# Kernel tuning notes

Measured on AMD Instinct MI355X. Metric: run time of the kernel, lower is better.

The kernel has to match this reference:

```python
import jax, jax.numpy as jnp
import numpy as np

H, NH, HD = 1024, 16, 64
B, T, S = 2, 1024, 3
NOISE, STEP, TEMP, NSTEPS = 0.1, 0.01, 1.0, 5
LN_EPS = 1e-5


def setup_inputs() -> dict:
    key = jax.random.key(0)
    ks = jax.random.split(key, 9)
    return {
        "queries": jax.random.normal(ks[0], (B, NH, T, HD), jnp.float32),
        "keys": jax.random.normal(ks[1], (B, NH, T, HD), jnp.float32),
        "values": jax.random.normal(ks[2], (B, NH, T, HD), jnp.float32),
        "hidden_states": jax.random.normal(ks[3], (B, T, H), jnp.float32),
        "W1": jax.random.normal(ks[4], (H, H), jnp.float32) * 0.02,
        "b1": jnp.zeros((H,), jnp.float32),
        "ln_g": jnp.ones((H,), jnp.float32),
        "ln_b": jnp.zeros((H,), jnp.float32),
        "W2": jax.random.normal(ks[5], (H, H), jnp.float32) * 0.02,
        "b2": jnp.zeros((H,), jnp.float32),
        "hyp_noise": jax.random.normal(ks[6], (S, B, NH, T, HD), jnp.float32),
        "ref_noise": jax.random.normal(ks[7], (S, NSTEPS - 1, B, NH, T, HD), jnp.float32),
    }


def _attention_energy(q, k, v):
    # q: [S,B,H,T,D]; k,v: [B,H,T,D] -> energy [S,B]
    scores = jnp.einsum('sbhtd,bhud->sbhtu', q, k) / jnp.sqrt(jnp.float32(q.shape[-1]))
    attn = jax.nn.softmax(scores, axis=-1)
    out = jnp.einsum('sbhtu,bhud->sbhtd', attn, v)
    out_mag = jnp.linalg.norm(out, axis=-1).mean(axis=(2, 3))          # [S,B]
    entropy = -(attn * jnp.log(attn + 1e-8)).sum(axis=-1).mean(axis=(2, 3))
    align = (q * k[None]).sum(axis=-1).mean(axis=(2, 3))
    return out_mag - 0.1 * entropy - 0.05 * align


def reference(queries, keys, values, hidden_states, W1, b1, ln_g, ln_b, W2, b2,
              hyp_noise, ref_noise):
    # query_predictor: Linear -> LayerNorm -> ReLU -> Linear
    x = hidden_states @ W1.T + b1
    mu = x.mean(axis=-1, keepdims=True)
    var = ((x - mu) ** 2).mean(axis=-1, keepdims=True)
    x = (x - mu) / jnp.sqrt(var + LN_EPS) * ln_g + ln_b
    x = jax.nn.relu(x)
    ctx = x @ W2.T + b2                                   # [B,T,H]
    ctx = ctx.reshape(B, T, NH, HD).transpose(0, 2, 1, 3) # [B,NH,T,HD]

    # exploration hypotheses, refined jointly over the sample axis
    q = queries[None] + hyp_noise * NOISE                 # [S,B,NH,T,HD]
    for step in range(NSTEPS):
        q = q - STEP * (q - ctx[None])                    # PCN prediction-error update
        if step < NSTEPS - 1:
            q = q + ref_noise[:, step] * 0.01

    energies = _attention_energy(q, keys, values)         # [S,B]
    probs = jax.nn.softmax(-energies / TEMP, axis=0)      # [S,B]
    selected = jnp.einsum('sb,sbhtd->bhtd', probs, q)     # softmax-weighted mix
    return selected, keys, values
```

## Files before the change

kernel.cpp:

```cpp
#include <hip/hip_runtime.h>
#include <hip/hip_bf16.h>
#include <math.h>

#define NB 2
#define NHH 16
#define TT 1024
#define HDD 64
#define NSS 3
#define HH 1024

typedef float f4 __attribute__((ext_vector_type(4)));
typedef short bf16x8 __attribute__((ext_vector_type(8)));
typedef unsigned short u16;
typedef u16 u16x4 __attribute__((ext_vector_type(4)));

__device__ inline u16 f2bf(float f) {
    union { float f; unsigned u; } v; v.f = f;
    unsigned r = (v.u + 0x7FFFu + ((v.u >> 16) & 1u)) >> 16;
    return (u16)r;
}
__device__ inline float bf2f(u16 u) {
    union { unsigned u; float f; } v; v.u = ((unsigned)u) << 16;
    return v.f;
}
__device__ inline unsigned cvtpk(float lo, float hi) {
    unsigned r;
    asm("v_cvt_pk_bf16_f32 %0, %1, %2" : "=v"(r) : "v"(lo), "v"(hi));
    return r;
}
__device__ inline void gl_lds16(const u16* g, u16* l) {
    __builtin_amdgcn_global_load_lds(
        (const __attribute__((address_space(1))) unsigned int*)g,
        (__attribute__((address_space(3))) unsigned int*)l, 16, 0, 0);
}

__device__ inline float red16sum(float v) {
    v += __shfl_xor(v, 1);
    v += __shfl_xor(v, 2);
    v += __shfl_xor(v, 4);
    v += __shfl_xor(v, 8);
    return v;
}
__device__ inline float red64sum(float v) {
    v += __shfl_xor(v, 1);
    v += __shfl_xor(v, 2);
    v += __shfl_xor(v, 4);
    v += __shfl_xor(v, 8);
    v += __shfl_xor(v, 16);
    v += __shfl_xor(v, 32);
    return v;
}

__global__ __launch_bounds__(256) void k_prep(const float* __restrict__ hs, u16* __restrict__ hs_b,
                                              const float* __restrict__ W1, u16* __restrict__ w1_b,
                                              const float* __restrict__ W2, u16* __restrict__ w2_b,
                                              const float* __restrict__ keys, u16* __restrict__ k_b,
                                              float* __restrict__ outk,
                                              const float* __restrict__ V, u16* __restrict__ vt_b,
                                              float* __restrict__ outv) {
    __shared__ float tile[64][65];
    int b = blockIdx.x;
    if (b < 4096) {
        const float* s; u16* d; int base;
        if (b < 2048)      { s = hs; d = hs_b; base = 0; }
        else if (b < 3072) { s = W1; d = w1_b; base = 2048; }
        else               { s = W2; d = w2_b; base = 3072; }
        int i = (b - base) * 256 + threadIdx.x;
        f4 v = ((const f4*)s)[i];
        u16x4 o;
        o[0] = f2bf(v[0]); o[1] = f2bf(v[1]); o[2] = f2bf(v[2]); o[3] = f2bf(v[3]);
        ((u16x4*)d)[i] = o;
        return;
    }
    if (b < 5120) {
        int c = (b - 4096) * 256 + threadIdx.x;
        int bh = c >> 13, t = (c >> 3) & 1023, col8 = c & 7;
        int kt = t >> 6, row = t & 63;
        const float* sp = keys + (size_t)c * 8;
        f4 v0 = *(const f4*)(sp);
        f4 v1 = *(const f4*)(sp + 4);
        *(f4*)(outk + (size_t)c * 8) = v0;
        *(f4*)(outk + (size_t)c * 8 + 4) = v1;
        union { unsigned u[4]; int4 i4; } o;
        o.u[0] = cvtpk(v0[0] * 0.125f, v0[1] * 0.125f);
        o.u[1] = cvtpk(v0[2] * 0.125f, v0[3] * 0.125f);
        o.u[2] = cvtpk(v1[0] * 0.125f, v1[1] * 0.125f);
        o.u[3] = cvtpk(v1[2] * 0.125f, v1[3] * 0.125f);
        *(int4*)(k_b + (size_t)(bh * 16 + kt) * 4096 + row * 64 + ((col8 ^ (row & 7)) << 3)) = o.i4;
        return;
    }
    int idx = b - 5120;
    int bh = idx >> 4, kt = idx & 15, t0 = kt * 64;
    int r = threadIdx.x >> 2, c0 = (threadIdx.x & 3) * 16;
    const float* vp = V + ((size_t)bh * TT + t0) * HDD;
#pragma unroll
    for (int j = 0; j < 16; j += 4) {
        f4 v = *(const f4*)(vp + r * HDD + c0 + j);
        tile[r][c0 + j + 0] = v[0]; tile[r][c0 + j + 1] = v[1];
        tile[r][c0 + j + 2] = v[2]; tile[r][c0 + j + 3] = v[3];
        *(f4*)(outv + ((size_t)bh * TT + t0 + r) * HDD + c0 + j) = v;
    }
    __syncthreads();
    int d = threadIdx.x >> 2, x0 = (threadIdx.x & 3) * 16;
    u16* op = vt_b + (size_t)(bh * 16 + kt) * 4096 + d * 64;
#pragma unroll
    for (int cc = 0; cc < 2; ++cc) {
        int c8 = (x0 >> 3) + cc;
        union { unsigned u[4]; int4 i4; } o;
#pragma unroll
        for (int p = 0; p < 4; ++p)
            o.u[p] = cvtpk(tile[c8 * 8 + 2 * p][d], tile[c8 * 8 + 2 * p + 1][d]);
        *(int4*)(op + ((c8 ^ (d & 7)) << 3)) = o.i4;
    }
}

template <int EPI>
__global__ __launch_bounds__(256) void k_gemm_bt(const u16* __restrict__ A,
                                                 const u16* __restrict__ Bm,
                                                 const float* __restrict__ bias,
                                                 const float* __restrict__ que,
                                                 void* __restrict__ outv) {
    const int K = 1024, N = 1024;
    int w = threadIdx.x >> 6, l = threadIdx.x & 63, lr = l & 15, lg = l >> 4;
    int m0 = blockIdx.y * 64 + w * 16;
    int n0 = blockIdx.x * 64;
    const u16* ap = A + (size_t)(m0 + lr) * K + lg * 8;
    const u16* bp = Bm + (size_t)(n0 + lr) * K + lg * 8;
    f4 z4 = {0.f, 0.f, 0.f, 0.f};
    f4 acc[4] = {z4, z4, z4, z4};
#pragma unroll 2
    for (int kk = 0; kk < K; kk += 32) {
        bf16x8 a  = *(const bf16x8*)(ap + kk);
        bf16x8 b0 = *(const bf16x8*)(bp + kk);
        bf16x8 b1 = *(const bf16x8*)(bp + 16 * K + kk);
        bf16x8 b2 = *(const bf16x8*)(bp + 32 * K + kk);
        bf16x8 b3 = *(const bf16x8*)(bp + 48 * K + kk);
        acc[0] = __builtin_amdgcn_mfma_f32_16x16x32_bf16(a, b0, acc[0], 0, 0, 0);
        acc[1] = __builtin_amdgcn_mfma_f32_16x16x32_bf16(a, b1, acc[1], 0, 0, 0);
        acc[2] = __builtin_amdgcn_mfma_f32_16x16x32_bf16(a, b2, acc[2], 0, 0, 0);
        acc[3] = __builtin_amdgcn_mfma_f32_16x16x32_bf16(a, b3, acc[3], 0, 0, 0);
    }
    const float A5 = 0.9509900499f, CC = 1.0f - A5;
#pragma unroll
    for (int cf = 0; cf < 4; ++cf) {
        int col = n0 + cf * 16 + lr;
        float bs = bias[col];
#pragma unroll
        for (int r = 0; r < 4; ++r) {
            int row = m0 + lg * 4 + r;
            float v = acc[cf][r] + bs;
            if (EPI == 0) {
                ((u16*)outv)[(size_t)row * N + col] = f2bf(v);
            } else {
                int b = row >> 10, t = row & 1023, nh = col >> 6, hd = col & 63;
                size_t oidx = (((size_t)(b * NHH + nh)) * TT + t) * HDD + hd;
                ((float*)outv)[oidx] = A5 * que[oidx] + CC * v;
            }
        }
    }
}

__global__ __launch_bounds__(256) void k_lnrelu(const u16* __restrict__ X,
                                                const float* __restrict__ g,
                                                const float* __restrict__ bta,
                                                u16* __restrict__ xr) {
    int row = blockIdx.x;
    u16x4 xv = ((const u16x4*)(X + (size_t)row * HH))[threadIdx.x];
    f4 v;
    v[0] = bf2f(xv[0]); v[1] = bf2f(xv[1]); v[2] = bf2f(xv[2]); v[3] = bf2f(xv[3]);
    float s = v[0] + v[1] + v[2] + v[3];
    float s2 = v[0] * v[0] + v[1] * v[1] + v[2] * v[2] + v[3] * v[3];
    s = red64sum(s);
    s2 = red64sum(s2);
    __shared__ float red[8];
    int w = threadIdx.x >> 6, l = threadIdx.x & 63;
    if (l == 0) { red[w] = s; red[w + 4] = s2; }
    __syncthreads();
    float S1 = red[0] + red[1] + red[2] + red[3];
    float S2 = red[4] + red[5] + red[6] + red[7];
    float mu = S1 * (1.0f / 1024.0f);
    float var = S2 * (1.0f / 1024.0f) - mu * mu;
    float rstd = rsqrtf(var + 1e-5f);
    f4 gv = ((const f4*)g)[threadIdx.x];
    f4 bv = ((const f4*)bta)[threadIdx.x];
    u16x4 o;
#pragma unroll
    for (int j = 0; j < 4; ++j) {
        float y = (v[j] - mu) * rstd * gv[j] + bv[j];
        y = fmaxf(y, 0.f);
        o[j] = f2bf(y);
    }
    ((u16x4*)(xr + (size_t)row * HH))[threadIdx.x] = o;
}

__global__ __launch_bounds__(256, 3) void k_attn(const float* __restrict__ basep_,
                                                 const float* __restrict__ hyp,
                                                 const float* __restrict__ rn,
                                                 const u16* __restrict__ Kb,
                                                 const u16* __restrict__ Vt,
                                                 u16* __restrict__ qq,
                                                 float* __restrict__ part) {
    int bi = blockIdx.x;
    int p_ = bi & 31, j_ = bi >> 5;
    int h = p_ & 15, b = p_ >> 4;
    int s = j_ >> 3, qt2 = j_ & 7;
    int sb = s * 2 + b;
    int bh = b * NHH + h;
    int pi = sb * 128 + h * 8 + qt2;
    int w = threadIdx.x >> 6, l = threadIdx.x & 63, lr = l & 15, lg = l >> 4;
    int t0 = qt2 * 128;
    f4 z4 = {0.f, 0.f, 0.f, 0.f};

    __shared__ u16 Ks[2][4096];
    __shared__ u16 Vs[2][4096];
    __shared__ u16 plds[8][1024];

    const u16* kT = Kb + (size_t)(bh * 16) * 4096;
    const u16* vT = Vt + (size_t)(bh * 16) * 4096;

#pragma unroll
    for (int j = 0; j < 2; ++j) {
        int co = (w + 4 * j) * 512;
        gl_lds16(kT + co + l * 8, &Ks[0][co]);
        gl_lds16(vT + co + l * 8, &Vs[0][co]);
    }

    const float CH = 0.1f * 0.9509900499f;
    const float C0 = 0.0096059601f, C1 = 0.0097029900f, C2 = 0.0098010000f, C3 = 0.0099f;
    const float* basep = basep_ + ((size_t)bh * TT) * HDD;
    const float* hypp = hyp + ((size_t)(sb * NHH + h) * TT) * HDD;
    const float* rn0p = rn + ((size_t)(((s * 4 + 0) * 2 + b) * NHH + h) * TT) * HDD;
    const float* rn1p = rn + ((size_t)(((s * 4 + 1) * 2 + b) * NHH + h) * TT) * HDD;
    const float* rn2p = rn + ((size_t)(((s * 4 + 2) * 2 + b) * NHH + h) * TT) * HDD;
    const float* rn3p = rn + ((size_t)(((s * 4 + 3) * 2 + b) * NHH + h) * TT) * HDD;
    u16* qqp = qq + ((size_t)(sb * NHH + h) * TT) * HDD;

    char* slab = (char*)&plds[0][0];
    {
        int t = threadIdx.x;
#pragma unroll
        for (int m = 0; m < 4; ++m) {
            int j = t + 256 * m;
            size_t off = (size_t)t0 * HDD + (size_t)j * 8;
            f4 a0 = *(const f4*)(basep + off);
            f4 a1 = *(const f4*)(basep + off + 4);
            a0 += CH * __builtin_nontemporal_load((const f4*)(hypp + off));
            a1 += CH * __builtin_nontemporal_load((const f4*)(hypp + off + 4));
            a0 += C0 * __builtin_nontemporal_load((const f4*)(rn0p + off));
            a1 += C0 * __builtin_nontemporal_load((const f4*)(rn0p + off + 4));
            a0 += C1 * __builtin_nontemporal_load((const f4*)(rn1p + off));
            a1 += C1 * __builtin_nontemporal_load((const f4*)(rn1p + off + 4));
            a0 += C2 * __builtin_nontemporal_load((const f4*)(rn2p + off));
            a1 += C2 * __builtin_nontemporal_load((const f4*)(rn2p + off + 4));
            a0 += C3 * __builtin_nontemporal_load((const f4*)(rn3p + off));
            a1 += C3 * __builtin_nontemporal_load((const f4*)(rn3p + off + 4));
            union { unsigned u[4]; int4 i4; } o;
            o.u[0] = cvtpk(a0[0], a0[1]); o.u[1] = cvtpk(a0[2], a0[3]);
            o.u[2] = cvtpk(a1[0], a1[1]); o.u[3] = cvtpk(a1[2], a1[3]);
            int row = j >> 3, slot = j & 7;
            *(int4*)(slab + row * 128 + (((slot ^ (row & 7))) << 4)) = o.i4;
            *(int4*)(qqp + (size_t)t0 * HDD + (size_t)j * 8) = o.i4;
        }
    }
    __syncthreads();

    bf16x8 aq[2][2];
#pragma unroll
    for (int qr = 0; qr < 2; ++qr) {
        int r_ = w * 32 + qr * 16 + lr;
#pragma unroll
        for (int c = 0; c < 2; ++c)
            aq[qr][c] = *(const bf16x8*)(slab + r_ * 128 + (((c * 4 + lg) ^ (r_ & 7)) << 4));
    }

    f4 acco[2][4] = {{z4, z4, z4, z4}, {z4, z4, z4, z4}};
    float zrow[2][4] = {{0.f, 0.f, 0.f, 0.f}, {0.f, 0.f, 0.f, 0.f}};
    float wrow[2][4] = {{0.f, 0.f, 0.f, 0.f}, {0.f, 0.f, 0.f, 0.f}};
    float al_lane = 0.f;
    int kdiag = qt2 * 2 + (w >> 1);

    for (int kt = 0; kt < 16; ++kt) {
        int cur = kt & 1;
        if (kt < 15) {
#pragma unroll
            for (int j = 0; j < 2; ++j) {
                int co = (w + 4 * j) * 512;
                gl_lds16(kT + (kt + 1) * 4096 + co + l * 8, &Ks[cur ^ 1][co]);
                gl_lds16(vT + (kt + 1) * 4096 + co + l * 8, &Vs[cur ^ 1][co]);
            }
        }
        char* KsB = (char*)Ks[cur];
        char* VsB = (char*)Vs[cur];

        f4 sc[2][4];
        __builtin_amdgcn_s_setprio(1);
#pragma unroll
        for (int cf = 0; cf < 4; ++cf) {
            int row = cf * 16 + lr, rs = row & 7;
            bf16x8 bk0 = *(const bf16x8*)(KsB + row * 128 + ((lg ^ rs) << 4));
            bf16x8 bk1 = *(const bf16x8*)(KsB + row * 128 + (((4 + lg) ^ rs) << 4));
            f4 t0a = __builtin_amdgcn_mfma_f32_16x16x32_bf16(aq[0][0], bk0, z4, 0, 0, 0);
            sc[0][cf] = __builtin_amdgcn_mfma_f32_16x16x32_bf16(aq[0][1], bk1, t0a, 0, 0, 0);
            f4 t1a = __builtin_amdgcn_mfma_f32_16x16x32_bf16(aq[1][0], bk0, z4, 0, 0, 0);
            sc[1][cf] = __builtin_amdgcn_mfma_f32_16x16x32_bf16(aq[1][1], bk1, t1a, 0, 0, 0);
        }
        __builtin_amdgcn_s_setprio(0);

        if (kt == kdiag) {
            f4 sd0 = (w & 1) ? sc[0][2] : sc[0][0];
            f4 sd1 = (w & 1) ? sc[1][3] : sc[1][1];
            int rr = lr & 3;
            float e0 = rr == 0 ? sd0[0] : (rr == 1 ? sd0[1] : (rr == 2 ? sd0[2] : sd0[3]));
            float e1 = rr == 0 ? sd1[0] : (rr == 1 ? sd1[1] : (rr == 2 ? sd1[2] : sd1[3]));
            if (lg == (lr >> 2)) al_lane += (e0 + e1) * 8.0f;
        }

#pragma unroll
        for (int qr = 0; qr < 2; ++qr) {
            u16* pl = &plds[w * 2 + qr][0];
#pragma unroll
            for (int cf = 0; cf < 4; ++cf) {
                float p0 = __expf(sc[qr][cf][0]);
                float p1 = __expf(sc[qr][cf][1]);
                float p2 = __expf(sc[qr][cf][2]);
                float p3 = __expf(sc[qr][cf][3]);
                zrow[qr][0] += p0; zrow[qr][1] += p1;
                zrow[qr][2] += p2; zrow[qr][3] += p3;
                wrow[qr][0] = fmaf(p0, sc[qr][cf][0], wrow[qr][0]);
                wrow[qr][1] = fmaf(p1, sc[qr][cf][1], wrow[qr][1]);
                wrow[qr][2] = fmaf(p2, sc[qr][cf][2], wrow[qr][2]);
                wrow[qr][3] = fmaf(p3, sc[qr][cf][3], wrow[qr][3]);
                unsigned pa01 = cvtpk(p0, p1), pa23 = cvtpk(p2, p3);
                int base_ = cf * 16 + lr;
                pl[(((lg * 4 + 0) * 64 + base_)) ^ (((lg * 4 + 0) & 7) << 3)] = (u16)pa01;
                pl[(((lg * 4 + 1) * 64 + base_)) ^ (((lg * 4 + 1) & 7) << 3)] = (u16)(pa01 >> 16);
                pl[(((lg * 4 + 2) * 64 + base_)) ^ (((lg * 4 + 2) & 7) << 3)] = (u16)pa23;
                pl[(((lg * 4 + 3) * 64 + base_)) ^ (((lg * 4 + 3) & 7) << 3)] = (u16)(pa23 >> 16);
            }
        }
        bf16x8 pa[2][2];
#pragma unroll
        for (int qr = 0; qr < 2; ++qr) {
            const u16* pl = &plds[w * 2 + qr][0];
            pa[qr][0] = *(const bf16x8*)&pl[(lr * 64 + lg * 8) ^ ((lr & 7) << 3)];
            pa[qr][1] = *(const bf16x8*)&pl[(lr * 64 + 32 + lg * 8) ^ ((lr & 7) << 3)];
        }
        __builtin_amdgcn_s_setprio(1);
#pragma unroll
        for (int cf = 0; cf < 4; ++cf) {
            int row = cf * 16 + lr, rs = row & 7;
            bf16x8 bv0 = *(const bf16x8*)(VsB + row * 128 + ((lg ^ rs) << 4));
            bf16x8 bv1 = *(const bf16x8*)(VsB + row * 128 + (((4 + lg) ^ rs) << 4));
            acco[0][cf] = __builtin_amdgcn_mfma_f32_16x16x32_bf16(pa[0][0], bv0, acco[0][cf], 0, 0, 0);
            acco[0][cf] = __builtin_amdgcn_mfma_f32_16x16x32_bf16(pa[0][1], bv1, acco[0][cf], 0, 0, 0);
            acco[1][cf] = __builtin_amdgcn_mfma_f32_16x16x32_bf16(pa[1][0], bv0, acco[1][cf], 0, 0, 0);
            acco[1][cf] = __builtin_amdgcn_mfma_f32_16x16x32_bf16(pa[1][1], bv1, acco[1][cf], 0, 0, 0);
        }
        __builtin_amdgcn_s_setprio(0);

        __syncthreads();
    }

    float magw = 0.f, entw = 0.f;
#pragma unroll
    for (int qr = 0; qr < 2; ++qr) {
#pragma unroll
        for (int r = 0; r < 4; ++r) {
            float zz = red16sum(zrow[qr][r]);
            float ww = red16sum(wrow[qr][r]);
            float ssq = acco[qr][0][r] * acco[qr][0][r] + acco[qr][1][r] * acco[qr][1][r] +
                        acco[qr][2][r] * acco[qr][2][r] + acco[qr][3][r] * acco[qr][3][r];
            ssq = red16sum(ssq);
            float inv = 1.0f / zz;
            magw += sqrtf(ssq) * inv;
            entw += __logf(zz) - ww * inv;
        }
    }
    magw += __shfl_xor(magw, 16); magw += __shfl_xor(magw, 32);
    entw += __shfl_xor(entw, 16); entw += __shfl_xor(entw, 32);
    float al = red64sum(al_lane);

    __shared__ float red[4][3];
    if (l == 0) { red[w][0] = magw; red[w][1] = entw; red[w][2] = al; }
    __syncthreads();
    if (threadIdx.x == 0) {
        part[pi * 3 + 0] = red[0][0] + red[1][0] + red[2][0] + red[3][0];
        part[pi * 3 + 1] = red[0][1] + red[1][1] + red[2][1] + red[3][1];
        part[pi * 3 + 2] = red[0][2] + red[1][2] + red[2][2] + red[3][2];
    }
}

__global__ void k_finalize(const float* __restrict__ part, float* __restrict__ probs) {
    int w = threadIdx.x >> 6, l = threadIdx.x & 63;
    __shared__ float eng[6];
    if (w < 6) {
        float a0 = 0.f, a1 = 0.f, a2 = 0.f;
        for (int i = l; i < 128; i += 64) {
            const float* pp = part + (size_t)(w * 128 + i) * 3;
            a0 += pp[0]; a1 += pp[1]; a2 += pp[2];
        }
        a0 = red64sum(a0); a1 = red64sum(a1); a2 = red64sum(a2);
        if (l == 0) {
            const float inv = 1.0f / 16384.0f;
            eng[w] = a0 * inv - 0.1f * (a1 * inv) - 0.05f * (a2 * inv);
        }
    }
    __syncthreads();
    if (threadIdx.x < 2) {
        int b = threadIdx.x;
        float e0 = -eng[0 + b], e1 = -eng[2 + b], e2 = -eng[4 + b];
        float mx = fmaxf(e0, fmaxf(e1, e2));
        float x0 = __expf(e0 - mx), x1 = __expf(e1 - mx), x2 = __expf(e2 - mx);
        float inv = 1.0f / (x0 + x1 + x2);
        probs[0 + b] = x0 * inv;
        probs[2 + b] = x1 * inv;
        probs[4 + b] = x2 * inv;
    }
}

__global__ __launch_bounds__(256) void k_select(const u16* __restrict__ qq,
                                                const float* __restrict__ probs,
                                                float* __restrict__ out) {
    const int NQ4 = 524288;
    int i = blockIdx.x * 256 + threadIdx.x;
    int b = i >> 18;
    float p0 = probs[0 + b], p1 = probs[2 + b], p2 = probs[4 + b];
    u16x4 a0 = ((const u16x4*)qq)[i];
    u16x4 a1 = ((const u16x4*)qq)[NQ4 + i];
    u16x4 a2 = ((const u16x4*)qq)[2 * NQ4 + i];
    f4 v;
#pragma unroll
    for (int j = 0; j < 4; ++j)
        v[j] = p0 * bf2f(a0[j]) + p1 * bf2f(a1[j]) + p2 * bf2f(a2[j]);
    ((f4*)out)[i] = v;
}

extern "C" void kernel_launch(void* const* d_in, const int* in_sizes, int n_in,
                              void* d_out, int out_size, void* d_ws, size_t ws_size,
                              hipStream_t stream) {
    const float* queries = (const float*)d_in[0];
    const float* keys    = (const float*)d_in[1];
    const float* values  = (const float*)d_in[2];
    const float* hs      = (const float*)d_in[3];
    const float* W1      = (const float*)d_in[4];
    const float* b1      = (const float*)d_in[5];
    const float* ln_g    = (const float*)d_in[6];
    const float* ln_b    = (const float*)d_in[7];
    const float* W2      = (const float*)d_in[8];
    const float* b2      = (const float*)d_in[9];
    const float* hyp     = (const float*)d_in[10];
    const float* rn      = (const float*)d_in[11];
    float* out = (float*)d_out;
    char* ws = (char*)d_ws;

    const size_t MB = 1024ull * 1024ull;
    u16*   qq16 = (u16*)(ws);
    u16*   hs_b = (u16*)(ws + 0 * MB);
    u16*   w1_b = (u16*)(ws + 4 * MB);
    u16*   w2_b = (u16*)(ws + 6 * MB);
    u16*   X    = (u16*)(ws + 8 * MB);
    u16*   xr   = (u16*)(ws + 16 * MB);
    float* base = (float*)(ws + 24 * MB);
    u16*   k_b  = (u16*)(ws + 32 * MB);
    u16*   vt_b = (u16*)(ws + 36 * MB);
    float* part = (float*)(ws + 40 * MB);
    float* probs= (float*)(ws + 40 * MB + 65536);

    k_prep<<<5632, 256, 0, stream>>>(hs, hs_b, W1, w1_b, W2, w2_b,
                                     keys, k_b, out + 2097152,
                                     values, vt_b, out + 4194304);

    k_gemm_bt<0><<<dim3(16, 32), 256, 0, stream>>>(hs_b, w1_b, b1, nullptr, X);
    k_lnrelu<<<2048, 256, 0, stream>>>(X, ln_g, ln_b, xr);
    k_gemm_bt<1><<<dim3(16, 32), 256, 0, stream>>>(xr, w2_b, b2, queries, base);

    k_attn<<<768, 256, 0, stream>>>(base, hyp, rn, k_b, vt_b, qq16, part);
    k_finalize<<<1, 384, 0, stream>>>(part, probs);
    k_select<<<2048, 256, 0, stream>>>(qq16, probs, out);
}
```

Measured before the change: 167.4 us.

## Precombine noise terms in prep kernel and rebuild hypotheses from base plus noise

The five noise tensors (hyp and four ref_noise steps) are combined once in k_prep into a single bf16 noise tensor per sample. k_attn then reads base plus one bf16 noise stream instead of five fp32 streams, and no longer writes the bf16 hypothesis buffer qq. k_select rebuilds the selected output as base + sum_s p_s*noise_s, using the fact that the probabilities sum to one. The aim is to cut the heavy fp32 noise traffic inside the attention kernel and remove the qq write. The cost is extra prep work and a change in rounding, since noise is rounded to bf16 separately from base.

```diff
diff --git a/kernel.cpp b/kernel.cpp
--- a/kernel.cpp
+++ b/kernel.cpp
@@ -51,7 +51,16 @@
     return v;
 }
 
-__global__ __launch_bounds__(256) void k_prep(const float* __restrict__ hs, u16* __restrict__ hs_b,
+#define PCN_CH 0.0950990050f
+#define PCN_C0 0.0096059601f
+#define PCN_C1 0.0097029900f
+#define PCN_C2 0.0098010000f
+#define PCN_C3 0.0099000000f
+
+__global__ __launch_bounds__(256) void k_prep(const float* __restrict__ hyp,
+                                              const float* __restrict__ rn,
+                                              u16* __restrict__ noise16,
+                                              const float* __restrict__ hs, u16* __restrict__ hs_b,
                                               const float* __restrict__ W1, u16* __restrict__ w1_b,
                                               const float* __restrict__ W2, u16* __restrict__ w2_b,
                                               const float* __restrict__ keys, u16* __restrict__ k_b,
@@ -60,20 +69,51 @@
                                               float* __restrict__ outv) {
     __shared__ float tile[64][65];
     int b = blockIdx.x;
-    if (b < 4096) {
+    if (b < 1536) {
+        int sidx = b >> 9, blk = b & 511;
+        size_t so = (size_t)sidx * 2097152;
+        int o = blk * 4096 + threadIdx.x * 4;
+        const float* hp = hyp + so;
+        const float* r0 = rn + (size_t)(sidx * 4 + 0) * 2097152;
+        const float* r1 = rn + (size_t)(sidx * 4 + 1) * 2097152;
+        const float* r2 = rn + (size_t)(sidx * 4 + 2) * 2097152;
+        const float* r3 = rn + (size_t)(sidx * 4 + 3) * 2097152;
+        u16* np = noise16 + so;
+        f4 vh[4], v0[4], v1[4], v2[4], v3[4];
+#pragma unroll
+        for (int j = 0; j < 4; ++j) {
+            vh[j] = __builtin_nontemporal_load((const f4*)(hp + o + j * 1024));
+            v0[j] = __builtin_nontemporal_load((const f4*)(r0 + o + j * 1024));
+            v1[j] = __builtin_nontemporal_load((const f4*)(r1 + o + j * 1024));
+            v2[j] = __builtin_nontemporal_load((const f4*)(r2 + o + j * 1024));
+            v3[j] = __builtin_nontemporal_load((const f4*)(r3 + o + j * 1024));
+        }
+#pragma unroll
+        for (int j = 0; j < 4; ++j) {
+            f4 v = PCN_CH * vh[j] + PCN_C0 * v0[j] + PCN_C1 * v1[j] +
+                   PCN_C2 * v2[j] + PCN_C3 * v3[j];
+            unsigned pr[2];
+            pr[0] = cvtpk(v[0], v[1]);
+            pr[1] = cvtpk(v[2], v[3]);
+            *(uint2*)(np + o + j * 1024) = *(uint2*)pr;
+        }
+        return;
+    }
+    if (b < 5632) {
+        int b2 = b - 1536;
         const float* s; u16* d; int base;
-        if (b < 2048)      { s = hs; d = hs_b; base = 0; }
-        else if (b < 3072) { s = W1; d = w1_b; base = 2048; }
-        else               { s = W2; d = w2_b; base = 3072; }
-        int i = (b - base) * 256 + threadIdx.x;
+        if (b2 < 2048)      { s = hs; d = hs_b; base = 0; }
+        else if (b2 < 3072) { s = W1; d = w1_b; base = 2048; }
+        else                { s = W2; d = w2_b; base = 3072; }
+        int i = (b2 - base) * 256 + threadIdx.x;
         f4 v = ((const f4*)s)[i];
         u16x4 o;
         o[0] = f2bf(v[0]); o[1] = f2bf(v[1]); o[2] = f2bf(v[2]); o[3] = f2bf(v[3]);
         ((u16x4*)d)[i] = o;
         return;
     }
-    if (b < 5120) {
-        int c = (b - 4096) * 256 + threadIdx.x;
+    if (b < 6656) {
+        int c = (b - 5632) * 256 + threadIdx.x;
         int bh = c >> 13, t = (c >> 3) & 1023, col8 = c & 7;
         int kt = t >> 6, row = t & 63;
         const float* sp = keys + (size_t)c * 8;
@@ -89,7 +129,7 @@
         *(int4*)(k_b + (size_t)(bh * 16 + kt) * 4096 + row * 64 + ((col8 ^ (row & 7)) << 3)) = o.i4;
         return;
     }
-    int idx = b - 5120;
+    int idx = b - 6656;
     int bh = idx >> 4, kt = idx & 15, t0 = kt * 64;
     int r = threadIdx.x >> 2, c0 = (threadIdx.x & 3) * 16;
     const float* vp = V + ((size_t)bh * TT + t0) * HDD;
@@ -194,11 +234,9 @@
 }
 
 __global__ __launch_bounds__(256, 3) void k_attn(const float* __restrict__ basep_,
-                                                 const float* __restrict__ hyp,
-                                                 const float* __restrict__ rn,
+                                                 const u16* __restrict__ noise16,
                                                  const u16* __restrict__ Kb,
                                                  const u16* __restrict__ Vt,
-                                                 u16* __restrict__ qq,
                                                  float* __restrict__ part) {
     int bi = blockIdx.x;
     int p_ = bi & 31, j_ = bi >> 5;
@@ -225,15 +263,8 @@
         gl_lds16(vT + co + l * 8, &Vs[0][co]);
     }
 
-    const float CH = 0.1f * 0.9509900499f;
-    const float C0 = 0.0096059601f, C1 = 0.0097029900f, C2 = 0.0098010000f, C3 = 0.0099f;
-    const float* basep = basep_ + ((size_t)bh * TT) * HDD;
-    const float* hypp = hyp + ((size_t)(sb * NHH + h) * TT) * HDD;
-    const float* rn0p = rn + ((size_t)(((s * 4 + 0) * 2 + b) * NHH + h) * TT) * HDD;
-    const float* rn1p = rn + ((size_t)(((s * 4 + 1) * 2 + b) * NHH + h) * TT) * HDD;
-    const float* rn2p = rn + ((size_t)(((s * 4 + 2) * 2 + b) * NHH + h) * TT) * HDD;
-    const float* rn3p = rn + ((size_t)(((s * 4 + 3) * 2 + b) * NHH + h) * TT) * HDD;
-    u16* qqp = qq + ((size_t)(sb * NHH + h) * TT) * HDD;
+    const float* basep = basep_ + (size_t)bh * TT * HDD;
+    const u16* noisep = noise16 + (size_t)s * 2097152 + (size_t)bh * TT * HDD;
 
     char* slab = (char*)&plds[0][0];
     {
@@ -244,22 +275,18 @@
             size_t off = (size_t)t0 * HDD + (size_t)j * 8;
             f4 a0 = *(const f4*)(basep + off);
             f4 a1 = *(const f4*)(basep + off + 4);
-            a0 += CH * __builtin_nontemporal_load((const f4*)(hypp + off));
-            a1 += CH * __builtin_nontemporal_load((const f4*)(hypp + off + 4));
-            a0 += C0 * __builtin_nontemporal_load((const f4*)(rn0p + off));
-            a1 += C0 * __builtin_nontemporal_load((const f4*)(rn0p + off + 4));
-            a0 += C1 * __builtin_nontemporal_load((const f4*)(rn1p + off));
-            a1 += C1 * __builtin_nontemporal_load((const f4*)(rn1p + off + 4));
-            a0 += C2 * __builtin_nontemporal_load((const f4*)(rn2p + off));
-            a1 += C2 * __builtin_nontemporal_load((const f4*)(rn2p + off + 4));
-            a0 += C3 * __builtin_nontemporal_load((const f4*)(rn3p + off));
-            a1 += C3 * __builtin_nontemporal_load((const f4*)(rn3p + off + 4));
+            union { int4 i4; u16 u[8]; } nv;
+            nv.i4 = *(const int4*)(noisep + off);
+#pragma unroll
+            for (int k = 0; k < 4; ++k) {
+                a0[k] += bf2f(nv.u[k]);
+                a1[k] += bf2f(nv.u[4 + k]);
+            }
             union { unsigned u[4]; int4 i4; } o;
             o.u[0] = cvtpk(a0[0], a0[1]); o.u[1] = cvtpk(a0[2], a0[3]);
             o.u[2] = cvtpk(a1[0], a1[1]); o.u[3] = cvtpk(a1[2], a1[3]);
             int row = j >> 3, slot = j & 7;
             *(int4*)(slab + row * 128 + (((slot ^ (row & 7))) << 4)) = o.i4;
-            *(int4*)(qqp + (size_t)t0 * HDD + (size_t)j * 8) = o.i4;
         }
     }
     __syncthreads();
@@ -418,20 +445,21 @@
     }
 }
 
-__global__ __launch_bounds__(256) void k_select(const u16* __restrict__ qq,
+__global__ __launch_bounds__(256) void k_select(const float* __restrict__ base,
+                                                const u16* __restrict__ noise16,
                                                 const float* __restrict__ probs,
                                                 float* __restrict__ out) {
-    const int NQ4 = 524288;
+    const int NG = 524288;
     int i = blockIdx.x * 256 + threadIdx.x;
     int b = i >> 18;
     float p0 = probs[0 + b], p1 = probs[2 + b], p2 = probs[4 + b];
-    u16x4 a0 = ((const u16x4*)qq)[i];
-    u16x4 a1 = ((const u16x4*)qq)[NQ4 + i];
-    u16x4 a2 = ((const u16x4*)qq)[2 * NQ4 + i];
-    f4 v;
+    f4 v = ((const f4*)base)[i];
+    u16x4 n0 = ((const u16x4*)noise16)[i];
+    u16x4 n1 = ((const u16x4*)noise16)[NG + i];
+    u16x4 n2 = ((const u16x4*)noise16)[2 * NG + i];
 #pragma unroll
     for (int j = 0; j < 4; ++j)
-        v[j] = p0 * bf2f(a0[j]) + p1 * bf2f(a1[j]) + p2 * bf2f(a2[j]);
+        v[j] += p0 * bf2f(n0[j]) + p1 * bf2f(n1[j]) + p2 * bf2f(n2[j]);
     ((f4*)out)[i] = v;
 }
 
@@ -454,19 +482,20 @@
     char* ws = (char*)d_ws;
 
     const size_t MB = 1024ull * 1024ull;
-    u16*   qq16 = (u16*)(ws);
-    u16*   hs_b = (u16*)(ws + 0 * MB);
-    u16*   w1_b = (u16*)(ws + 4 * MB);
-    u16*   w2_b = (u16*)(ws + 6 * MB);
-    u16*   X    = (u16*)(ws + 8 * MB);
-    u16*   xr   = (u16*)(ws + 16 * MB);
-    float* base = (float*)(ws + 24 * MB);
-    u16*   k_b  = (u16*)(ws + 32 * MB);
-    u16*   vt_b = (u16*)(ws + 36 * MB);
-    float* part = (float*)(ws + 40 * MB);
-    float* probs= (float*)(ws + 40 * MB + 65536);
-
-    k_prep<<<5632, 256, 0, stream>>>(hs, hs_b, W1, w1_b, W2, w2_b,
+    u16*   hs_b  = (u16*)(ws + 0 * MB);
+    u16*   w1_b  = (u16*)(ws + 4 * MB);
+    u16*   w2_b  = (u16*)(ws + 6 * MB);
+    u16*   X     = (u16*)(ws + 8 * MB);
+    u16*   xr    = (u16*)(ws + 12 * MB);
+    u16*   n16   = (u16*)(ws + 16 * MB);
+    float* base  = (float*)(ws + 28 * MB);
+    u16*   k_b   = (u16*)(ws + 36 * MB);
+    u16*   vt_b  = (u16*)(ws + 40 * MB);
+    float* part  = (float*)(ws + 44 * MB);
+    float* probs = (float*)(ws + 44 * MB + 65536);
+
+    k_prep<<<7168, 256, 0, stream>>>(hyp, rn, n16,
+                                     hs, hs_b, W1, w1_b, W2, w2_b,
                                      keys, k_b, out + 2097152,
                                      values, vt_b, out + 4194304);
 
@@ -474,7 +503,7 @@
     k_lnrelu<<<2048, 256, 0, stream>>>(X, ln_g, ln_b, xr);
     k_gemm_bt<1><<<dim3(16, 32), 256, 0, stream>>>(xr, w2_b, b2, queries, base);
 
-    k_attn<<<768, 256, 0, stream>>>(base, hyp, rn, k_b, vt_b, qq16, part);
+    k_attn<<<768, 256, 0, stream>>>(base, n16, k_b, vt_b, part);
     k_finalize<<<1, 384, 0, stream>>>(part, probs);
-    k_select<<<2048, 256, 0, stream>>>(qq16, probs, out);
-}
+    k_select<<<2048, 256, 0, stream>>>(base, n16, probs, out);
+}
```

Result: no change. 169.6 us (+1.3%).
